# Kernel optimization log

Measured on AMD Instinct MI355X. Metric: run time of the kernel, lower is better.

Reference implementation:

```python
import jax, jax.numpy as jnp
import numpy as np

B, N, D, H, FF, K, L = 8, 4096, 128, 8, 512, 16, 2
DH = D // H
EPS = 1e-5


def setup_inputs() -> dict:
    key = jax.random.key(0)
    ks = jax.random.split(key, 32)
    s = 0.02
    inp = {
        "x": jax.random.normal(ks[0], (B, N, 8), dtype=jnp.float32),
        "xyz_w": jax.random.normal(ks[1], (D, 3), jnp.float32) * s,
        "xyz_b": jnp.zeros((D,), jnp.float32),
        "ohe_w": jax.random.normal(ks[2], (D, 5), jnp.float32) * s,
        "ohe_b": jnp.zeros((D,), jnp.float32),
        # per-layer transformer params stacked on leading L axis
        "in_proj_w": jax.random.normal(ks[3], (L, 3 * D, D), jnp.float32) * s,
        "in_proj_b": jnp.zeros((L, 3 * D), jnp.float32),
        "out_proj_w": jax.random.normal(ks[4], (L, D, D), jnp.float32) * s,
        "out_proj_b": jnp.zeros((L, D), jnp.float32),
        "ln1_w": jnp.ones((L, D), jnp.float32),
        "ln1_b": jnp.zeros((L, D), jnp.float32),
        "lin1_w": jax.random.normal(ks[5], (L, FF, D), jnp.float32) * s,
        "lin1_b": jnp.zeros((L, FF), jnp.float32),
        "lin2_w": jax.random.normal(ks[6], (L, D, FF), jnp.float32) * s,
        "lin2_b": jnp.zeros((L, D), jnp.float32),
        "ln2_w": jnp.ones((L, D), jnp.float32),
        "ln2_b": jnp.zeros((L, D), jnp.float32),
        "fc1_w": jax.random.normal(ks[7], (FF, D), jnp.float32) * s,
        "fc1_b": jnp.zeros((FF,), jnp.float32),
        "fc2_w": jax.random.normal(ks[8], (1, FF), jnp.float32) * s,
        "fc2_b": jnp.zeros((1,), jnp.float32),
    }
    return inp


def _layer_norm(x, w, b):
    m = jnp.mean(x, -1, keepdims=True)
    v = jnp.mean((x - m) ** 2, -1, keepdims=True)
    return (x - m) * jax.lax.rsqrt(v + EPS) * w + b


def _knn_attention(xyz, feat):
    # squared euclidean distances preserve top-k ordering of cdist(p=2)
    d2 = jnp.sum((xyz[:, :, None, :] - xyz[:, None, :, :]) ** 2, -1)  # [B,N,N]
    _, idx = jax.lax.top_k(-d2, K + 1)  # ascending distance
    idx = idx[..., 1:]  # drop self -> [B,N,K]
    knn = jax.vmap(lambda f, i: f[i])(feat, idx)  # [B,N,K,D]
    scale = 1.0 / np.sqrt(D)
    scores = jnp.einsum('bnd,bnkd->bnk', feat, knn) * scale
    w = jax.nn.softmax(scores, -1)
    return jnp.einsum('bnk,bnkd->bnd', w, knn)


def _mha(x, in_w, in_b, out_w, out_b):
    qkv = x @ in_w.T + in_b  # [B,N,3D]
    q, k, v = jnp.split(qkv, 3, axis=-1)
    def heads(t):
        return t.reshape(B, N, H, DH).transpose(0, 2, 1, 3)  # [B,H,N,DH]
    q, k, v = heads(q), heads(k), heads(v)
    scores = jnp.einsum('bhqd,bhkd->bhqk', q, k) / np.sqrt(DH)
    a = jax.nn.softmax(scores, -1)
    o = jnp.einsum('bhqk,bhkd->bhqd', a, v).transpose(0, 2, 1, 3).reshape(B, N, D)
    return o @ out_w.T + out_b


def reference(x, xyz_w, xyz_b, ohe_w, ohe_b, in_proj_w, in_proj_b, out_proj_w,
              out_proj_b, ln1_w, ln1_b, lin1_w, lin1_b, lin2_w, lin2_b,
              ln2_w, ln2_b, fc1_w, fc1_b, fc2_w, fc2_b):
    xyz = x[:, :, :3]
    ohe = x[:, :, 3:8]
    feat = (xyz @ xyz_w.T + xyz_b) + (ohe @ ohe_w.T + ohe_b)  # [B,N,D]
    h = _knn_attention(xyz, feat)
    # post-norm TransformerEncoder (PyTorch default, relu, no dropout at eval)
    for l in range(L):
        a = _mha(h, in_proj_w[l], in_proj_b[l], out_proj_w[l], out_proj_b[l])
        h = _layer_norm(h + a, ln1_w[l], ln1_b[l])
        f = jax.nn.relu(h @ lin1_w[l].T + lin1_b[l]) @ lin2_w[l].T + lin2_b[l]
        h = _layer_norm(h + f, ln2_w[l], ln2_b[l])
    pooled = jnp.mean(h, axis=1)  # [B,D]
    out = jax.nn.sigmoid(jax.nn.relu(pooled @ fc1_w.T + fc1_b) @ fc2_w.T + fc2_b)
    return out
```

## Files before the change

kernel.cpp:

```cpp
#include <hip/hip_runtime.h>

#define Bq 8
#define Nq 4096
#define Dq 128
#define Hq 8
#define FFq 512
#define KNNq 16
#define Lq 2
#define DHq 16
#define EPSq 1e-5f

typedef _Float16 half4 __attribute__((ext_vector_type(4)));
typedef _Float16 half2t __attribute__((ext_vector_type(2)));
typedef float v4f __attribute__((ext_vector_type(4)));

static __device__ __forceinline__ half2t pkrtz(float a, float b) {
    return __builtin_bit_cast(half2t, __builtin_amdgcn_cvt_pkrtz(a, b));
}

__global__ void wcvt_kernel(const float* __restrict__ ipw, const float* __restrict__ opw,
                            const float* __restrict__ l1w, const float* __restrict__ l2w,
                            _Float16* __restrict__ wb) {
    int i = blockIdx.x * 256 + threadIdx.x;
    float v;
    if (i < 98304) v = ipw[i];
    else if (i < 131072) v = opw[i - 98304];
    else if (i < 262144) v = l1w[i - 131072];
    else v = l2w[i - 262144];
    wb[i] = (_Float16)v;
}

__global__ void feat_kernel(const float* __restrict__ x, const float* __restrict__ xyz_w,
                            const float* __restrict__ xyz_b, const float* __restrict__ ohe_w,
                            const float* __restrict__ ohe_b, _Float16* __restrict__ feat16) {
    int i = blockIdx.x * blockDim.x + threadIdx.x;
    if (i >= Bq * Nq * Dq) return;
    int d = i & 127;
    int t = i >> 7;
    const float* xr = x + (size_t)t * 8;
    float s = xyz_b[d] + ohe_b[d];
    s += xr[0] * xyz_w[d * 3 + 0] + xr[1] * xyz_w[d * 3 + 1] + xr[2] * xyz_w[d * 3 + 2];
    s += xr[3] * ohe_w[d * 5 + 0] + xr[4] * ohe_w[d * 5 + 1] + xr[5] * ohe_w[d * 5 + 2]
       + xr[6] * ohe_w[d * 5 + 3] + xr[7] * ohe_w[d * 5 + 4];
    feat16[i] = (_Float16)s;
}

__global__ __launch_bounds__(256) void knn_kernel(const float* __restrict__ x, int* __restrict__ idx) {
    __shared__ __attribute__((aligned(16))) float sxyz[Nq][4];
    __shared__ unsigned int md[256][16];
    int b = blockIdx.y;
    int tid = threadIdx.x;
    for (int p = tid; p < Nq; p += 256) {
        const float* xr = x + ((size_t)b * Nq + p) * 8;
        float4 v = make_float4(xr[0], xr[1], xr[2], 0.f);
        *(float4*)&sxyz[p][0] = v;
    }
    __syncthreads();
    int qi = tid >> 3;
    int part = tid & 7;
    int n = blockIdx.x * 32 + qi;
    float qx = sxyz[n][0], qy = sxyz[n][1], qz = sxyz[n][2];
    unsigned int bd[KNNq];
#pragma unroll
    for (int i = 0; i < KNNq; i++) bd[i] = 0xFFFFFFFFu;
    int j0 = part * 512;
    int rot = part * 2;
#pragma unroll 2
    for (int jj = 0; jj < 512; jj++) {
        int j = j0 + ((jj + rot) & 511);
        float4 p4 = *(const float4*)&sxyz[j][0];
        float dx = qx - p4.x, dy = qy - p4.y, dz = qz - p4.z;
        float d2 = fmaf(dx, dx, fmaf(dy, dy, dz * dz));
        unsigned int key = (__float_as_uint(d2) & 0xFFFFF000u) | (unsigned int)j;
        key = (j == n) ? 0xFFFFFFFFu : key;
#pragma unroll
        for (int i = 0; i < KNNq; i++) {
            unsigned int lo = bd[i] < key ? bd[i] : key;
            unsigned int hi = bd[i] < key ? key : bd[i];
            bd[i] = lo; key = hi;
        }
    }
#pragma unroll
    for (int i = 0; i < KNNq; i++) md[tid][i] = bd[i];
    __syncthreads();
    if (part == 0) {
        unsigned int pall = 0;
        int* op = idx + ((size_t)b * Nq + n) * KNNq;
        int base_row = qi * 8;
#pragma unroll
        for (int s = 0; s < KNNq; s++) {
            unsigned int best = 0xFFFFFFFFu; int bp = 0;
#pragma unroll
            for (int p2 = 0; p2 < 8; p2++) {
                unsigned int ptr = (pall >> (p2 * 4)) & 15u;
                unsigned int v = md[base_row + p2][ptr];
                if (v < best) { best = v; bp = p2; }
            }
            op[s] = (int)(best & 4095u);
            pall += (1u << (bp * 4));
        }
    }
}

__global__ __launch_bounds__(256, 4) void knn_attn_kernel(const _Float16* __restrict__ feat16,
                                                          const int* __restrict__ idx,
                                                          float* __restrict__ h,
                                                          _Float16* __restrict__ h16) {
    int wave = threadIdx.x >> 6;
    int lane = threadIdx.x & 63;
    int token = blockIdx.x * 4 + wave;
    int b = token >> 12;
    half2t fh = ((const half2t*)(feat16 + (size_t)token * Dq))[lane];
    float2 f = make_float2((float)fh[0], (float)fh[1]);
    const int* ip = idx + (size_t)token * KNNq;
    int jj[KNNq];
#pragma unroll
    for (int k = 0; k < KNNq; k++) jj[k] = ip[k];
    float2 g[KNNq];
#pragma unroll
    for (int k = 0; k < KNNq; k++) {
        half2t gh = ((const half2t*)(feat16 + (((size_t)b << 12) + jj[k]) * Dq))[lane];
        g[k] = make_float2((float)gh[0], (float)gh[1]);
    }
    float sc[KNNq];
#pragma unroll
    for (int k = 0; k < KNNq; k++) {
        float p = f.x * g[k].x + f.y * g[k].y;
#pragma unroll
        for (int m = 1; m < 64; m <<= 1) p += __shfl_xor(p, m);
        sc[k] = p * 0.088388347648318447f;
    }
    float mx = sc[0];
#pragma unroll
    for (int k = 1; k < KNNq; k++) mx = fmaxf(mx, sc[k]);
    float sum = 0.f;
#pragma unroll
    for (int k = 0; k < KNNq; k++) { sc[k] = __expf(sc[k] - mx); sum += sc[k]; }
    float inv = 1.f / sum;
    float o0 = 0.f, o1 = 0.f;
#pragma unroll
    for (int k = 0; k < KNNq; k++) { o0 += sc[k] * g[k].x; o1 += sc[k] * g[k].y; }
    o0 *= inv; o1 *= inv;
    ((float2*)(h + (size_t)token * Dq))[lane] = make_float2(o0, o1);
    ((half2t*)(h16 + (size_t)token * Dq))[lane] = pkrtz(o0, o1);
}

template <int MODE>
__global__ __launch_bounds__(256) void hgemm_kernel(const _Float16* __restrict__ A,
                                                    const _Float16* __restrict__ W,
                                                    const float* __restrict__ bias,
                                                    void* __restrict__ Cout,
                                                    int M, int Nc, int K) {
    int tid = threadIdx.x;
    int lane = tid & 63, w = tid >> 6;
    int l15 = lane & 15, l4 = lane >> 4;
    int m0 = blockIdx.y * 64 + w * 16;
    int n0 = blockIdx.x * 64;
    const _Float16* Ap = A + (size_t)(m0 + l15) * K + l4 * 4;
    const _Float16* Wp = W + (size_t)(n0 + l15) * K + l4 * 4;
    v4f acc[4] = {{0.f, 0.f, 0.f, 0.f}, {0.f, 0.f, 0.f, 0.f}, {0.f, 0.f, 0.f, 0.f}, {0.f, 0.f, 0.f, 0.f}};
    for (int ks = 0; ks < K; ks += 16) {
        half4 af = *(const half4*)(Ap + ks);
#pragma unroll
        for (int nt = 0; nt < 4; nt++) {
            half4 wf = *(const half4*)(Wp + (size_t)nt * 16 * K + ks);
            acc[nt] = __builtin_amdgcn_mfma_f32_16x16x16f16(wf, af, acc[nt], 0, 0, 0);
        }
    }
    int m = m0 + l15;
#pragma unroll
    for (int nt = 0; nt < 4; nt++) {
        int nb = n0 + nt * 16 + l4 * 4;
        float4 bv = *(const float4*)(bias + nb);
        float v0 = acc[nt][0] + bv.x, v1 = acc[nt][1] + bv.y;
        float v2 = acc[nt][2] + bv.z, v3 = acc[nt][3] + bv.w;
        int n_base = n0 + nt * 16;
        int sel = n_base >> 7;
        if (MODE == 2 && sel == 0) {
            v0 *= 0.36067376f; v1 *= 0.36067376f; v2 *= 0.36067376f; v3 *= 0.36067376f;
        }
        half2t lo = pkrtz(v0, v1);
        half2t hi = pkrtz(v2, v3);
        half4 hv; hv[0] = lo[0]; hv[1] = lo[1]; hv[2] = hi[0]; hv[3] = hi[1];
        if (sel < 2) {
            int hh = (n_base >> 4) & 7;
            size_t base = (size_t)sel * (64ull * Nq * 16)
                        + ((size_t)((m >> 12) * 8 + hh)) * (Nq * 16)
                        + (size_t)(m & 4095) * 16 + l4 * 4;
            *(half4*)((_Float16*)Cout + base) = hv;
        } else {
            int hh = (n_base >> 4) & 7;
            size_t vb = 2ull * 64 * Nq * 16
                      + ((size_t)((m >> 12) * 8 + hh)) * (16 * Nq)
                      + (size_t)(m & 4095);
            _Float16* vp = (_Float16*)Cout + vb + (size_t)(l4 * 4) * Nq;
            vp[0 * Nq] = hv[0]; vp[1 * Nq] = hv[1]; vp[2 * Nq] = hv[2]; vp[3 * Nq] = hv[3];
        }
    }
}

__global__ __launch_bounds__(256) void flash7_kernel(const _Float16* __restrict__ pk,
                                                     _Float16* __restrict__ out16) {
    __shared__ _Float16 Ks[2][64 * 20];
    __shared__ _Float16 Vs[2][16 * 66];
    int tid = threadIdx.x;
    int lane = tid & 63, w = tid >> 6;
    int bh = blockIdx.y;
    const _Float16* Qb = pk + (size_t)bh * (Nq * 16);
    const _Float16* Kb = pk + (size_t)(64 + bh) * (Nq * 16);
    const _Float16* Vt = pk + 2ull * 64 * Nq * 16 + (size_t)bh * (16 * Nq);
    int q0 = blockIdx.x * 64 + w * 16;
    int l15 = lane & 15, l4 = lane >> 4;

    half4 qf = *(const half4*)(Qb + (size_t)(q0 + l15) * 16 + l4 * 4);
    half4 ones; ones[0] = (_Float16)1.f; ones[1] = (_Float16)1.f; ones[2] = (_Float16)1.f; ones[3] = (_Float16)1.f;

    int sr = tid >> 2, sc = tid & 3;
    int vd = tid >> 4, vj = (tid & 15) * 4;
    const _Float16* Kg = Kb + (size_t)sr * 16 + sc * 4;
    const _Float16* Vg = Vt + (size_t)vd * Nq + vj;

    *(half4*)(Ks[0] + sr * 20 + sc * 4) = *(const half4*)(Kg);
    *(half4*)(Vs[0] + vd * 66 + vj) = *(const half4*)(Vg);
    __syncthreads();

    v4f o = {0.f, 0.f, 0.f, 0.f};
    v4f ls = {0.f, 0.f, 0.f, 0.f};

    for (int kt = 0; kt < Nq / 64; kt++) {
        int cur = kt & 1, nxt = cur ^ 1;
        if (kt < Nq / 64 - 1) {
            *(half4*)(Ks[nxt] + sr * 20 + sc * 4) = *(const half4*)(Kg + (size_t)(kt + 1) * 64 * 16);
            *(half4*)(Vs[nxt] + vd * 66 + vj) = *(const half4*)(Vg + (kt + 1) * 64);
        }
        v4f S[4];
#pragma unroll
        for (int g = 0; g < 4; g++) {
            half4 kf = *(const half4*)(Ks[cur] + (g * 16 + l15) * 20 + l4 * 4);
            S[g] = __builtin_amdgcn_mfma_f32_16x16x16f16(kf, qf, (v4f){0.f, 0.f, 0.f, 0.f}, 0, 0, 0);
        }
        half4 P[4];
#pragma unroll
        for (int g = 0; g < 4; g++) {
            float p0 = __builtin_amdgcn_exp2f(S[g][0]);
            float p1 = __builtin_amdgcn_exp2f(S[g][1]);
            float p2 = __builtin_amdgcn_exp2f(S[g][2]);
            float p3 = __builtin_amdgcn_exp2f(S[g][3]);
            half2t lo = pkrtz(p0, p1);
            half2t hi = pkrtz(p2, p3);
            P[g][0] = lo[0]; P[g][1] = lo[1]; P[g][2] = hi[0]; P[g][3] = hi[1];
        }
#pragma unroll
        for (int g = 0; g < 4; g++) {
            half4 vf = *(const half4*)(Vs[cur] + l15 * 66 + g * 16 + l4 * 4);
            o = __builtin_amdgcn_mfma_f32_16x16x16f16(vf, P[g], o, 0, 0, 0);
            ls = __builtin_amdgcn_mfma_f32_16x16x16f16(ones, P[g], ls, 0, 0, 0);
        }
        __syncthreads();
    }
    float inv = 1.f / ls[0];
    int row = q0 + l15;
    int b = bh >> 3, hh = bh & 7;
    half2t lo = pkrtz(o[0] * inv, o[1] * inv);
    half2t hi = pkrtz(o[2] * inv, o[3] * inv);
    half4 hv; hv[0] = lo[0]; hv[1] = lo[1]; hv[2] = hi[0]; hv[3] = hi[1];
    *(half4*)(out16 + ((size_t)(b * Nq + row)) * Dq + hh * 16 + l4 * 4) = hv;
}

__global__ __launch_bounds__(256) void hgemm_ln_kernel(const _Float16* __restrict__ A,
                                                       const _Float16* __restrict__ W,
                                                       const float* __restrict__ bias,
                                                       const float* __restrict__ lnw,
                                                       const float* __restrict__ lnb,
                                                       float* __restrict__ h,
                                                       _Float16* __restrict__ h16,
                                                       int K) {
    int tid = threadIdx.x;
    int lane = tid & 63, w = tid >> 6;
    int l15 = lane & 15, l4 = lane >> 4;
    int m0 = blockIdx.x * 64 + w * 16;
    const _Float16* Ap = A + (size_t)(m0 + l15) * K + l4 * 4;
    const _Float16* Wp = W + (size_t)l15 * K + l4 * 4;
    v4f acc[8] = {};
    for (int ks = 0; ks < K; ks += 16) {
        half4 af = *(const half4*)(Ap + ks);
#pragma unroll
        for (int nt = 0; nt < 8; nt++) {
            half4 wf = *(const half4*)(Wp + (size_t)nt * 16 * K + ks);
            acc[nt] = __builtin_amdgcn_mfma_f32_16x16x16f16(wf, af, acc[nt], 0, 0, 0);
        }
    }
    int m = m0 + l15;
    float x[8][4];
    float psum = 0.f;
#pragma unroll
    for (int nt = 0; nt < 8; nt++) {
        int nb = nt * 16 + l4 * 4;
        float4 bv = *(const float4*)(bias + nb);
        half4 rv = *(const half4*)(h16 + (size_t)m * Dq + nb);
        x[nt][0] = acc[nt][0] + bv.x + (float)rv[0];
        x[nt][1] = acc[nt][1] + bv.y + (float)rv[1];
        x[nt][2] = acc[nt][2] + bv.z + (float)rv[2];
        x[nt][3] = acc[nt][3] + bv.w + (float)rv[3];
        psum += (x[nt][0] + x[nt][1]) + (x[nt][2] + x[nt][3]);
    }
    psum += __shfl_xor(psum, 16);
    psum += __shfl_xor(psum, 32);
    float mean = psum * (1.f / 128.f);
    float vsum = 0.f;
#pragma unroll
    for (int nt = 0; nt < 8; nt++)
#pragma unroll
        for (int r = 0; r < 4; r++) {
            x[nt][r] -= mean;
            vsum += x[nt][r] * x[nt][r];
        }
    vsum += __shfl_xor(vsum, 16);
    vsum += __shfl_xor(vsum, 32);
    float inv = rsqrtf(vsum * (1.f / 128.f) + EPSq);
#pragma unroll
    for (int nt = 0; nt < 8; nt++) {
        int nb = nt * 16 + l4 * 4;
        float4 wv = *(const float4*)(lnw + nb);
        float4 bb = *(const float4*)(lnb + nb);
        float y0 = x[nt][0] * inv * wv.x + bb.x;
        float y1 = x[nt][1] * inv * wv.y + bb.y;
        float y2 = x[nt][2] * inv * wv.z + bb.z;
        float y3 = x[nt][3] * inv * wv.w + bb.w;
        *(float4*)(h + (size_t)m * Dq + nb) = make_float4(y0, y1, y2, y3);
        half2t lo = pkrtz(y0, y1);
        half2t hi = pkrtz(y2, y3);
        half4 hv2; hv2[0] = lo[0]; hv2[1] = lo[1]; hv2[2] = hi[0]; hv2[3] = hi[1];
        *(half4*)(h16 + (size_t)m * Dq + nb) = hv2;
    }
}

__global__ __launch_bounds__(256) void ffn_kernel(const _Float16* __restrict__ h16in,
                                                  const _Float16* __restrict__ W1,
                                                  const float* __restrict__ b1,
                                                  const _Float16* __restrict__ W2,
                                                  const float* __restrict__ b2,
                                                  const float* __restrict__ lnw,
                                                  const float* __restrict__ lnb,
                                                  float* __restrict__ h,
                                                  _Float16* __restrict__ h16) {
    int tid = threadIdx.x;
    int lane = tid & 63, w = tid >> 6;
    int l15 = lane & 15, l4 = lane >> 4;
    int m0 = blockIdx.x * 64 + w * 16;
    int m = m0 + l15;
    const _Float16* Ap = h16in + (size_t)m * Dq + l4 * 4;
    half4 afr[8];
#pragma unroll
    for (int t = 0; t < 8; t++) afr[t] = *(const half4*)(Ap + t * 16);
    half4 mid[32];
#pragma unroll
    for (int c = 0; c < 8; c++) {
        v4f acc[4] = {};
#pragma unroll
        for (int t = 0; t < 8; t++) {
#pragma unroll
            for (int nt = 0; nt < 4; nt++) {
                half4 wf = *(const half4*)(W1 + (size_t)(c * 64 + nt * 16 + l15) * 128 + t * 16 + l4 * 4);
                acc[nt] = __builtin_amdgcn_mfma_f32_16x16x16f16(wf, afr[t], acc[nt], 0, 0, 0);
            }
        }
#pragma unroll
        for (int nt = 0; nt < 4; nt++) {
            float4 bv = *(const float4*)(b1 + c * 64 + nt * 16 + l4 * 4);
            float v0 = fmaxf(acc[nt][0] + bv.x, 0.f);
            float v1 = fmaxf(acc[nt][1] + bv.y, 0.f);
            float v2 = fmaxf(acc[nt][2] + bv.z, 0.f);
            float v3 = fmaxf(acc[nt][3] + bv.w, 0.f);
            half2t lo = pkrtz(v0, v1), hi = pkrtz(v2, v3);
            half4 hv; hv[0] = lo[0]; hv[1] = lo[1]; hv[2] = hi[0]; hv[3] = hi[1];
            mid[c * 4 + nt] = hv;
        }
    }
    v4f acc8[8] = {};
#pragma unroll 4
    for (int t = 0; t < 32; t++) {
#pragma unroll
        for (int nt = 0; nt < 8; nt++) {
            half4 wf = *(const half4*)(W2 + (size_t)(nt * 16 + l15) * 512 + t * 16 + l4 * 4);
            acc8[nt] = __builtin_amdgcn_mfma_f32_16x16x16f16(wf, mid[t], acc8[nt], 0, 0, 0);
        }
    }
    float x[8][4];
    float psum = 0.f;
#pragma unroll
    for (int nt = 0; nt < 8; nt++) {
        int nb = nt * 16 + l4 * 4;
        float4 bv = *(const float4*)(b2 + nb);
        x[nt][0] = acc8[nt][0] + bv.x + (float)afr[nt][0];
        x[nt][1] = acc8[nt][1] + bv.y + (float)afr[nt][1];
        x[nt][2] = acc8[nt][2] + bv.z + (float)afr[nt][2];
        x[nt][3] = acc8[nt][3] + bv.w + (float)afr[nt][3];
        psum += (x[nt][0] + x[nt][1]) + (x[nt][2] + x[nt][3]);
    }
    psum += __shfl_xor(psum, 16);
    psum += __shfl_xor(psum, 32);
    float mean = psum * (1.f / 128.f);
    float vsum = 0.f;
#pragma unroll
    for (int nt = 0; nt < 8; nt++)
#pragma unroll
        for (int r = 0; r < 4; r++) {
            x[nt][r] -= mean;
            vsum += x[nt][r] * x[nt][r];
        }
    vsum += __shfl_xor(vsum, 16);
    vsum += __shfl_xor(vsum, 32);
    float inv = rsqrtf(vsum * (1.f / 128.f) + EPSq);
#pragma unroll
    for (int nt = 0; nt < 8; nt++) {
        int nb = nt * 16 + l4 * 4;
        float4 wv = *(const float4*)(lnw + nb);
        float4 bb = *(const float4*)(lnb + nb);
        float y0 = x[nt][0] * inv * wv.x + bb.x;
        float y1 = x[nt][1] * inv * wv.y + bb.y;
        float y2 = x[nt][2] * inv * wv.z + bb.z;
        float y3 = x[nt][3] * inv * wv.w + bb.w;
        *(float4*)(h + (size_t)m * Dq + nb) = make_float4(y0, y1, y2, y3);
        half2t lo = pkrtz(y0, y1);
        half2t hi = pkrtz(y2, y3);
        half4 hv2; hv2[0] = lo[0]; hv2[1] = lo[1]; hv2[2] = hi[0]; hv2[3] = hi[1];
        *(half4*)(h16 + (size_t)m * Dq + nb) = hv2;
    }
}

__global__ void pool_kernel(const float* __restrict__ h, float* __restrict__ part) {
    int c = blockIdx.x, b = blockIdx.y, d = threadIdx.x;
    const float* p = h + ((size_t)b * Nq + c * 256) * Dq + d;
    float s = 0.f;
    for (int n = 0; n < 256; n++) s += p[(size_t)n * Dq];
    part[((size_t)b * 16 + c) * Dq + d] = s;
}

__global__ __launch_bounds__(512) void head_kernel(const float* __restrict__ part,
                                                   const float* __restrict__ fc1_w, const float* __restrict__ fc1_b,
                                                   const float* __restrict__ fc2_w, const float* __restrict__ fc2_b,
                                                   float* __restrict__ out) {
    __shared__ float psh[Dq];
    __shared__ float red[512];
    int b = blockIdx.x, f = threadIdx.x;
    if (f < Dq) {
        float s = 0.f;
        for (int c = 0; c < 16; c++) s += part[((size_t)b * 16 + c) * Dq + f];
        psh[f] = s * (1.f / 4096.f);
    }
    __syncthreads();
    const float* wr = fc1_w + (size_t)f * Dq;
    float s = fc1_b[f];
    for (int d = 0; d < Dq; d++) s += psh[d] * wr[d];
    red[f] = fmaxf(s, 0.f) * fc2_w[f];
    __syncthreads();
    for (int st = 256; st > 0; st >>= 1) {
        if (f < st) red[f] += red[f + st];
        __syncthreads();
    }
    if (f == 0) out[b] = 1.f / (1.f + __expf(-(red[0] + fc2_b[0])));
}

extern "C" void kernel_launch(void* const* d_in, const int* in_sizes, int n_in,
                              void* d_out, int out_size, void* d_ws, size_t ws_size,
                              hipStream_t stream) {
    const float* x        = (const float*)d_in[0];
    const float* xyz_w    = (const float*)d_in[1];
    const float* xyz_b    = (const float*)d_in[2];
    const float* ohe_w    = (const float*)d_in[3];
    const float* ohe_b    = (const float*)d_in[4];
    const float* in_proj_w  = (const float*)d_in[5];
    const float* in_proj_b  = (const float*)d_in[6];
    const float* out_proj_w = (const float*)d_in[7];
    const float* out_proj_b = (const float*)d_in[8];
    const float* ln1_w    = (const float*)d_in[9];
    const float* ln1_b    = (const float*)d_in[10];
    const float* lin1_w   = (const float*)d_in[11];
    const float* lin1_b   = (const float*)d_in[12];
    const float* lin2_w   = (const float*)d_in[13];
    const float* lin2_b   = (const float*)d_in[14];
    const float* ln2_w    = (const float*)d_in[15];
    const float* ln2_b    = (const float*)d_in[16];
    const float* fc1_w    = (const float*)d_in[17];
    const float* fc1_b    = (const float*)d_in[18];
    const float* fc2_w    = (const float*)d_in[19];
    const float* fc2_b    = (const float*)d_in[20];
    float* outp = (float*)d_out;

    char* ws = (char*)d_ws;
    size_t off = 0;
    auto alloc = [&](size_t bytes) { void* p = ws + off; off += (bytes + 255) & ~255ULL; return p; };
    _Float16*  feat16 = (_Float16*)alloc((size_t)Bq * Nq * Dq * 2);
    float*     h      = (float*)alloc((size_t)Bq * Nq * Dq * 4);
    _Float16*  h16    = (_Float16*)alloc((size_t)Bq * Nq * Dq * 2);
    _Float16*  abuf16 = (_Float16*)alloc((size_t)Bq * Nq * Dq * 2);
    _Float16*  pkb    = (_Float16*)alloc(3ull * 64 * Nq * 16 * 2);
    _Float16*  wb     = (_Float16*)alloc(393216ull * 2);
    int*       idx    = (int*)alloc((size_t)Bq * Nq * KNNq * 4);
    float*     part   = (float*)alloc((size_t)Bq * 16 * Dq * 4);
    if (off > ws_size) return;

    const _Float16* wip16 = wb;
    const _Float16* wop16 = wb + 98304;
    const _Float16* wl116 = wb + 131072;
    const _Float16* wl216 = wb + 262144;

    int M = Bq * Nq;

    wcvt_kernel<<<1536, 256, 0, stream>>>(in_proj_w, out_proj_w, lin1_w, lin2_w, wb);
    feat_kernel<<<(Bq * Nq * Dq + 255) / 256, 256, 0, stream>>>(x, xyz_w, xyz_b, ohe_w, ohe_b, feat16);
    knn_kernel<<<dim3(Nq / 32, Bq), 256, 0, stream>>>(x, idx);
    knn_attn_kernel<<<M / 4, 256, 0, stream>>>(feat16, idx, h, h16);

    for (int l = 0; l < Lq; l++) {
        hgemm_kernel<2><<<dim3(384 / 64, M / 64), 256, 0, stream>>>(
            h16, wip16 + (size_t)l * 384 * 128, in_proj_b + l * 384, pkb, M, 384, 128);
        flash7_kernel<<<dim3(Nq / 64, Bq * Hq), 256, 0, stream>>>(pkb, abuf16);
        hgemm_ln_kernel<<<M / 64, 256, 0, stream>>>(
            abuf16, wop16 + (size_t)l * 128 * 128, out_proj_b + l * 128,
            ln1_w + l * 128, ln1_b + l * 128, h, h16, 128);
        ffn_kernel<<<M / 64, 256, 0, stream>>>(
            h16, wl116 + (size_t)l * 512 * 128, lin1_b + l * 512,
            wl216 + (size_t)l * 128 * 512, lin2_b + l * 128,
            ln2_w + l * 128, ln2_b + l * 128, h, h16);
    }

    pool_kernel<<<dim3(16, Bq), 128, 0, stream>>>(h, part);
    head_kernel<<<Bq, 512, 0, stream>>>(part, fc1_w, fc1_b, fc2_w, fc2_b, outp);
}
```

Baseline: 1.148 ms.

## Drop fp32 residual buffer, fuse pooling into last FFN, dual-list KNN

Stops writing the fp32 copy of h in the knn-attn, out-proj+LN and FFN kernels, keeping only the fp16 activations. The residual path presumably now reads the fp16 copy. The final FFN layer reduces its rows into per-wave partial sums, which removes the separate pool kernel and its full read of h. The KNN scan also keeps two independent sorted candidate lists that are merged at the end, giving more instruction-level parallelism in the insertion chain. Saving memory traffic costs some precision in the residual path and adds register pressure in the KNN kernel.

```diff
diff --git a/kernel.cpp b/kernel.cpp
--- a/kernel.cpp
+++ b/kernel.cpp
@@ -60,28 +60,46 @@
     int part = tid & 7;
     int n = blockIdx.x * 32 + qi;
     float qx = sxyz[n][0], qy = sxyz[n][1], qz = sxyz[n][2];
-    unsigned int bd[KNNq];
-#pragma unroll
-    for (int i = 0; i < KNNq; i++) bd[i] = 0xFFFFFFFFu;
+    unsigned int bdA[KNNq], bdB[KNNq];
+#pragma unroll
+    for (int i = 0; i < KNNq; i++) { bdA[i] = 0xFFFFFFFFu; bdB[i] = 0xFFFFFFFFu; }
     int j0 = part * 512;
     int rot = part * 2;
-#pragma unroll 2
-    for (int jj = 0; jj < 512; jj++) {
-        int j = j0 + ((jj + rot) & 511);
-        float4 p4 = *(const float4*)&sxyz[j][0];
-        float dx = qx - p4.x, dy = qy - p4.y, dz = qz - p4.z;
-        float d2 = fmaf(dx, dx, fmaf(dy, dy, dz * dz));
-        unsigned int key = (__float_as_uint(d2) & 0xFFFFF000u) | (unsigned int)j;
-        key = (j == n) ? 0xFFFFFFFFu : key;
+    for (int jj = 0; jj < 256; jj++) {
+        int j1 = j0 + ((jj + rot) & 511);
+        int j2 = j0 + ((jj + 256 + rot) & 511);
+        float4 p1 = *(const float4*)&sxyz[j1][0];
+        float4 p2 = *(const float4*)&sxyz[j2][0];
+        float dx1 = qx - p1.x, dy1 = qy - p1.y, dz1 = qz - p1.z;
+        float dx2 = qx - p2.x, dy2 = qy - p2.y, dz2 = qz - p2.z;
+        float d21 = fmaf(dx1, dx1, fmaf(dy1, dy1, dz1 * dz1));
+        float d22 = fmaf(dx2, dx2, fmaf(dy2, dy2, dz2 * dz2));
+        unsigned int k1 = (__float_as_uint(d21) & 0xFFFFF000u) | (unsigned int)j1;
+        unsigned int k2 = (__float_as_uint(d22) & 0xFFFFF000u) | (unsigned int)j2;
+        k1 = (j1 == n) ? 0xFFFFFFFFu : k1;
+        k2 = (j2 == n) ? 0xFFFFFFFFu : k2;
 #pragma unroll
         for (int i = 0; i < KNNq; i++) {
-            unsigned int lo = bd[i] < key ? bd[i] : key;
-            unsigned int hi = bd[i] < key ? key : bd[i];
-            bd[i] = lo; key = hi;
-        }
-    }
-#pragma unroll
-    for (int i = 0; i < KNNq; i++) md[tid][i] = bd[i];
+            unsigned int loA = bdA[i] < k1 ? bdA[i] : k1;
+            unsigned int hiA = bdA[i] < k1 ? k1 : bdA[i];
+            bdA[i] = loA; k1 = hiA;
+            unsigned int loB = bdB[i] < k2 ? bdB[i] : k2;
+            unsigned int hiB = bdB[i] < k2 ? k2 : bdB[i];
+            bdB[i] = loB; k2 = hiB;
+        }
+    }
+#pragma unroll
+    for (int t = 0; t < KNNq; t++) {
+        unsigned int key = bdB[t];
+#pragma unroll
+        for (int i = 0; i < KNNq; i++) {
+            unsigned int lo = bdA[i] < key ? bdA[i] : key;
+            unsigned int hi = bdA[i] < key ? key : bdA[i];
+            bdA[i] = lo; key = hi;
+        }
+    }
+#pragma unroll
+    for (int i = 0; i < KNNq; i++) md[tid][i] = bdA[i];
     __syncthreads();
     if (part == 0) {
         unsigned int pall = 0;
@@ -104,7 +122,6 @@
 
 __global__ __launch_bounds__(256, 4) void knn_attn_kernel(const _Float16* __restrict__ feat16,
                                                           const int* __restrict__ idx,
-                                                          float* __restrict__ h,
                                                           _Float16* __restrict__ h16) {
     int wave = threadIdx.x >> 6;
     int lane = threadIdx.x & 63;
@@ -140,9 +157,7 @@
     float o0 = 0.f, o1 = 0.f;
 #pragma unroll
     for (int k = 0; k < KNNq; k++) { o0 += sc[k] * g[k].x; o1 += sc[k] * g[k].y; }
-    o0 *= inv; o1 *= inv;
-    ((float2*)(h + (size_t)token * Dq))[lane] = make_float2(o0, o1);
-    ((half2t*)(h16 + (size_t)token * Dq))[lane] = pkrtz(o0, o1);
+    ((half2t*)(h16 + (size_t)token * Dq))[lane] = pkrtz(o0 * inv, o1 * inv);
 }
 
 template <int MODE>
@@ -272,7 +287,6 @@
                                                        const float* __restrict__ bias,
                                                        const float* __restrict__ lnw,
                                                        const float* __restrict__ lnb,
-                                                       float* __restrict__ h,
                                                        _Float16* __restrict__ h16,
                                                        int K) {
     int tid = threadIdx.x;
@@ -327,7 +341,6 @@
         float y1 = x[nt][1] * inv * wv.y + bb.y;
         float y2 = x[nt][2] * inv * wv.z + bb.z;
         float y3 = x[nt][3] * inv * wv.w + bb.w;
-        *(float4*)(h + (size_t)m * Dq + nb) = make_float4(y0, y1, y2, y3);
         half2t lo = pkrtz(y0, y1);
         half2t hi = pkrtz(y2, y3);
         half4 hv2; hv2[0] = lo[0]; hv2[1] = lo[1]; hv2[2] = hi[0]; hv2[3] = hi[1];
@@ -335,6 +348,7 @@
     }
 }
 
+template <int LAST>
 __global__ __launch_bounds__(256) void ffn_kernel(const _Float16* __restrict__ h16in,
                                                   const _Float16* __restrict__ W1,
                                                   const float* __restrict__ b1,
@@ -342,8 +356,8 @@
                                                   const float* __restrict__ b2,
                                                   const float* __restrict__ lnw,
                                                   const float* __restrict__ lnb,
-                                                  float* __restrict__ h,
-                                                  _Float16* __restrict__ h16) {
+                                                  _Float16* __restrict__ h16,
+                                                  float* __restrict__ part) {
     int tid = threadIdx.x;
     int lane = tid & 63, w = tid >> 6;
     int l15 = lane & 15, l4 = lane >> 4;
@@ -417,24 +431,38 @@
         int nb = nt * 16 + l4 * 4;
         float4 wv = *(const float4*)(lnw + nb);
         float4 bb = *(const float4*)(lnb + nb);
-        float y0 = x[nt][0] * inv * wv.x + bb.x;
-        float y1 = x[nt][1] * inv * wv.y + bb.y;
-        float y2 = x[nt][2] * inv * wv.z + bb.z;
-        float y3 = x[nt][3] * inv * wv.w + bb.w;
-        *(float4*)(h + (size_t)m * Dq + nb) = make_float4(y0, y1, y2, y3);
-        half2t lo = pkrtz(y0, y1);
-        half2t hi = pkrtz(y2, y3);
-        half4 hv2; hv2[0] = lo[0]; hv2[1] = lo[1]; hv2[2] = hi[0]; hv2[3] = hi[1];
-        *(half4*)(h16 + (size_t)m * Dq + nb) = hv2;
-    }
-}
-
-__global__ void pool_kernel(const float* __restrict__ h, float* __restrict__ part) {
-    int c = blockIdx.x, b = blockIdx.y, d = threadIdx.x;
-    const float* p = h + ((size_t)b * Nq + c * 256) * Dq + d;
-    float s = 0.f;
-    for (int n = 0; n < 256; n++) s += p[(size_t)n * Dq];
-    part[((size_t)b * 16 + c) * Dq + d] = s;
+        x[nt][0] = x[nt][0] * inv * wv.x + bb.x;
+        x[nt][1] = x[nt][1] * inv * wv.y + bb.y;
+        x[nt][2] = x[nt][2] * inv * wv.z + bb.z;
+        x[nt][3] = x[nt][3] * inv * wv.w + bb.w;
+        if (!LAST) {
+            half2t lo = pkrtz(x[nt][0], x[nt][1]);
+            half2t hi = pkrtz(x[nt][2], x[nt][3]);
+            half4 hv2; hv2[0] = lo[0]; hv2[1] = lo[1]; hv2[2] = hi[0]; hv2[3] = hi[1];
+            *(half4*)(h16 + (size_t)m * Dq + nb) = hv2;
+        }
+    }
+    if (LAST) {
+#pragma unroll
+        for (int nt = 0; nt < 8; nt++)
+#pragma unroll
+            for (int r = 0; r < 4; r++) {
+                float v = x[nt][r];
+                v += __shfl_xor(v, 1);
+                v += __shfl_xor(v, 2);
+                v += __shfl_xor(v, 4);
+                v += __shfl_xor(v, 8);
+                x[nt][r] = v;
+            }
+        if (l15 == 0) {
+            float* pp = part + ((size_t)blockIdx.x * 4 + w) * Dq;
+#pragma unroll
+            for (int nt = 0; nt < 8; nt++)
+#pragma unroll
+                for (int r = 0; r < 4; r++)
+                    pp[nt * 16 + l4 * 4 + r] = x[nt][r];
+        }
+    }
 }
 
 __global__ __launch_bounds__(512) void head_kernel(const float* __restrict__ part,
@@ -446,7 +474,7 @@
     int b = blockIdx.x, f = threadIdx.x;
     if (f < Dq) {
         float s = 0.f;
-        for (int c = 0; c < 16; c++) s += part[((size_t)b * 16 + c) * Dq + f];
+        for (int c = 0; c < 256; c++) s += part[((size_t)b * 256 + c) * Dq + f];
         psh[f] = s * (1.f / 4096.f);
     }
     __syncthreads();
@@ -492,13 +520,12 @@
     size_t off = 0;
     auto alloc = [&](size_t bytes) { void* p = ws + off; off += (bytes + 255) & ~255ULL; return p; };
     _Float16*  feat16 = (_Float16*)alloc((size_t)Bq * Nq * Dq * 2);
-    float*     h      = (float*)alloc((size_t)Bq * Nq * Dq * 4);
     _Float16*  h16    = (_Float16*)alloc((size_t)Bq * Nq * Dq * 2);
     _Float16*  abuf16 = (_Float16*)alloc((size_t)Bq * Nq * Dq * 2);
     _Float16*  pkb    = (_Float16*)alloc(3ull * 64 * Nq * 16 * 2);
     _Float16*  wb     = (_Float16*)alloc(393216ull * 2);
     int*       idx    = (int*)alloc((size_t)Bq * Nq * KNNq * 4);
-    float*     part   = (float*)alloc((size_t)Bq * 16 * Dq * 4);
+    float*     part   = (float*)alloc(2048ull * Dq * 4);
     if (off > ws_size) return;
 
     const _Float16* wip16 = wb;
@@ -511,7 +538,7 @@
     wcvt_kernel<<<1536, 256, 0, stream>>>(in_proj_w, out_proj_w, lin1_w, lin2_w, wb);
     feat_kernel<<<(Bq * Nq * Dq + 255) / 256, 256, 0, stream>>>(x, xyz_w, xyz_b, ohe_w, ohe_b, feat16);
     knn_kernel<<<dim3(Nq / 32, Bq), 256, 0, stream>>>(x, idx);
-    knn_attn_kernel<<<M / 4, 256, 0, stream>>>(feat16, idx, h, h16);
+    knn_attn_kernel<<<M / 4, 256, 0, stream>>>(feat16, idx, h16);
 
     for (int l = 0; l < Lq; l++) {
         hgemm_kernel<2><<<dim3(384 / 64, M / 64), 256, 0, stream>>>(
@@ -519,13 +546,17 @@
         flash7_kernel<<<dim3(Nq / 64, Bq * Hq), 256, 0, stream>>>(pkb, abuf16);
         hgemm_ln_kernel<<<M / 64, 256, 0, stream>>>(
             abuf16, wop16 + (size_t)l * 128 * 128, out_proj_b + l * 128,
-            ln1_w + l * 128, ln1_b + l * 128, h, h16, 128);
-        ffn_kernel<<<M / 64, 256, 0, stream>>>(
-            h16, wl116 + (size_t)l * 512 * 128, lin1_b + l * 512,
-            wl216 + (size_t)l * 128 * 512, lin2_b + l * 128,
-            ln2_w + l * 128, ln2_b + l * 128, h, h16);
-    }
-
-    pool_kernel<<<dim3(16, Bq), 128, 0, stream>>>(h, part);
+            ln1_w + l * 128, ln1_b + l * 128, h16, 128);
+        if (l == 0) {
+            ffn_kernel<0><<<M / 64, 256, 0, stream>>>(
+                h16, wl116, lin1_b, wl216, lin2_b, ln2_w, ln2_b, h16, part);
+        } else {
+            ffn_kernel<1><<<M / 64, 256, 0, stream>>>(
+                h16, wl116 + (size_t)l * 512 * 128, lin1_b + l * 512,
+                wl216 + (size_t)l * 128 * 512, lin2_b + l * 128,
+                ln2_w + l * 128, ln2_b + l * 128, h16, part);
+        }
+    }
+
     head_kernel<<<Bq, 512, 0, stream>>>(part, fc1_w, fc1_b, fc2_w, fc2_b, outp);
 }
```

Result: no change. 1.143 ms (-0.4%).
